# Optimization experiments

Measured on AMD Instinct MI355X. Metric: run time of the kernel, lower is better.

Reference implementation:

```python
import jax, jax.numpy as jnp
import numpy as np

B, T, N, E = 4, 8, 512, 8192
CIN, H, HEADS = 64, 128, 4


def setup_inputs() -> dict:
    key = jax.random.key(0)
    ks = jax.random.split(key, 8)
    G = B * T
    s = 0.05
    return {
        "x": jax.random.normal(ks[0], (G, N, CIN), jnp.float32),
        "edge_index": jax.random.randint(ks[1], (G, 2, E), 0, N, dtype=jnp.int64),
        "W1": jax.random.normal(ks[2], (CIN, H), jnp.float32) * s,
        "b1": jnp.zeros((H,), jnp.float32),
        "W2": jax.random.normal(ks[3], (H, H), jnp.float32) * s,
        "b2": jnp.zeros((H,), jnp.float32),
        "in_proj_w": jax.random.normal(ks[4], (3 * H, H), jnp.float32) * s,
        "in_proj_b": jnp.zeros((3 * H,), jnp.float32),
        "out_proj_w": jax.random.normal(ks[5], (H, H), jnp.float32) * s,
        "out_proj_b": jnp.zeros((H,), jnp.float32),
    }


def gcn_layer(x, src, dst, W, b, num_nodes):
    # PyG GCNConv: add self-loops, sym-normalize deg^-1/2[src]*deg^-1/2[dst]
    xl = x @ W                                            # [GN, H]
    deg = jax.ops.segment_sum(jnp.ones_like(dst, dtype=xl.dtype), dst,
                              num_segments=num_nodes) + 1.0  # +1 self-loop
    dinv = jax.lax.rsqrt(deg)
    norm = dinv[src] * dinv[dst]                          # [Etot]
    agg = jax.ops.segment_sum(xl[src] * norm[:, None], dst, num_segments=num_nodes)
    agg = agg + xl * (dinv * dinv)[:, None]               # self-loop term
    return agg + b


def reference(x, edge_index, W1, b1, W2, b2, in_proj_w, in_proj_b, out_proj_w, out_proj_b):
    G, n, cin = x.shape
    GN = G * n
    offs = (jnp.arange(G, dtype=edge_index.dtype) * n)[:, None]  # disjoint union
    src = (edge_index[:, 0, :] + offs).reshape(-1)
    dst = (edge_index[:, 1, :] + offs).reshape(-1)
    xf = x.reshape(GN, cin)
    h = gcn_layer(xf, src, dst, W1, b1, GN)
    h = gcn_layer(h, src, dst, W2, b2, GN)
    hc = h.shape[-1]
    h = h.reshape(B, T * n, hc)                           # [B, S, H]
    # torch.nn.MultiheadAttention with packed qkv in_proj
    qkv = h @ in_proj_w.T + in_proj_b
    q, k, v = jnp.split(qkv, 3, axis=-1)
    hd = hc // HEADS
    def sh(t):
        return t.reshape(B, -1, HEADS, hd).transpose(0, 2, 1, 3)  # [B,h,S,d]
    q, k, v = sh(q), sh(k), sh(v)
    att = jax.nn.softmax(jnp.einsum('bhqd,bhkd->bhqk', q, k) / jnp.sqrt(jnp.float32(hd)), axis=-1)
    o = jnp.einsum('bhqk,bhkd->bhqd', att, v).transpose(0, 2, 1, 3).reshape(B, -1, hc)
    return o @ out_proj_w.T + out_proj_b
```

## Files before the change

kernel.cpp:

```cpp
#include <hip/hip_runtime.h>
#include <hip/hip_bf16.h>

#define G     32
#define NPG   512
#define EPG   8192
#define GN    16384
#define ETOT  (G*EPG)
#define CIN   64
#define H     128
#define NB    4
#define S     4096
#define HEADS 4
#define HD    32
#define QKV   384

typedef __attribute__((ext_vector_type(8))) short short8;
typedef __attribute__((ext_vector_type(4))) float floatx4;

__device__ __forceinline__ float bf16_to_f32(unsigned short u) {
    unsigned int x = ((unsigned int)u) << 16;
    return __uint_as_float(x);
}
__device__ __forceinline__ unsigned short f32_to_bf16(float f) {
    __hip_bfloat16 h = (__hip_bfloat16)f;
    return *(unsigned short*)&h;
}
__device__ __forceinline__ float ldf(const void* p, long i, int f32) {
    return f32 ? ((const float*)p)[i] : bf16_to_f32(((const unsigned short*)p)[i]);
}

__global__ void detect_kernel(const unsigned short* __restrict__ xraw,
                              const int* __restrict__ eiraw, int* __restrict__ flags) {
    __shared__ float smax[256];
    __shared__ int   sor[256];
    int t = threadIdx.x;
    float m = 0.f;
    for (int i = t; i < 4096; i += 256)
        m = fmaxf(m, fabsf(bf16_to_f32(xraw[i])));
    int orv = 0;
    for (int i = t; i < 2048; i += 256)
        orv |= eiraw[2 * i + 1];
    smax[t] = m; sor[t] = orv;
    __syncthreads();
    for (int off = 128; off > 0; off >>= 1) {
        if (t < off) {
            smax[t] = fmaxf(smax[t], smax[t + off]);
            sor[t] |= sor[t + off];
        }
        __syncthreads();
    }
    if (t == 0) {
        flags[0] = (smax[0] > 1000.f) ? 1 : 0;
        flags[1] = (sor[0] == 0) ? 1 : 0;
    }
}

__global__ __launch_bounds__(NPG) void csr_kernel(const int* __restrict__ ei,
        const int* __restrict__ flags, int* __restrict__ cnt_g,
        int* __restrict__ row_start_g, float* __restrict__ dinv_g,
        int* __restrict__ csr_src) {
    __shared__ int cs[NPG], ctmp[NPG], fpos[NPG];
    int g = blockIdx.x, t = threadIdx.x;
    int sh = flags[1];
    cs[t] = 0;
    __syncthreads();
    const size_t sbase = ((size_t)(g * 2 + 0) * EPG) << sh;
    const size_t dbase = ((size_t)(g * 2 + 1) * EPG) << sh;
    for (int e = t; e < EPG; e += NPG)
        atomicAdd(&cs[ei[dbase + ((size_t)e << sh)]], 1);
    __syncthreads();
    int c = cs[t];
    ctmp[t] = c;
    __syncthreads();
    for (int off = 1; off < NPG; off <<= 1) {
        int v = (t >= off) ? ctmp[t - off] : 0;
        __syncthreads();
        ctmp[t] += v;
        __syncthreads();
    }
    int rs = g * EPG + ctmp[t] - c;
    fpos[t] = rs;
    cnt_g[g * NPG + t] = c;
    row_start_g[g * NPG + t] = rs;
    dinv_g[g * NPG + t] = 1.0f / sqrtf((float)c + 1.0f);
    __syncthreads();
    for (int e = t; e < EPG; e += NPG) {
        int s = ei[sbase + ((size_t)e << sh)];
        int d = ei[dbase + ((size_t)e << sh)];
        int pos = atomicAdd(&fpos[d], 1);
        csr_src[pos] = g * NPG + s;
    }
}

#define XN   (GN*CIN)
#define E1   (XN + H*CIN)
#define E2   (E1 + H*H)
#define E3   (E2 + QKV*H)
#define E4   (E3 + H*H)
#define E5   (E4 + H)
#define E6   (E5 + H)
#define E7   (E6 + QKV)
#define CTOT (E7 + H)
__global__ void conv_all_kernel(const void* x_raw, const void* W1_raw, const void* b1_raw,
                                const void* W2_raw, const void* b2_raw, const void* Wq_raw,
                                const void* bq_raw, const void* Wo_raw, const void* bo_raw,
                                unsigned short* __restrict__ xb,
                                unsigned short* __restrict__ W1T,
                                unsigned short* __restrict__ W2T,
                                unsigned short* __restrict__ Wqb,
                                unsigned short* __restrict__ Wob,
                                float* __restrict__ b1f, float* __restrict__ b2f,
                                float* __restrict__ bqf, float* __restrict__ bof,
                                const float* __restrict__ dinv,
                                const int* __restrict__ flags) {
    int i = blockIdx.x * blockDim.x + threadIdx.x;
    if (i >= CTOT) return;
    int f32 = flags[0];
    if (i < XN) {
        xb[i] = f32_to_bf16(ldf(x_raw, i, f32) * dinv[i >> 6]);
    } else if (i < E1) {
        int j = i - XN, c = j / CIN, r = j - c * CIN;
        W1T[j] = f32_to_bf16(ldf(W1_raw, (long)r * H + c, f32));
    } else if (i < E2) {
        int j = i - E1, c = j >> 7, r = j & 127;
        W2T[j] = f32_to_bf16(ldf(W2_raw, (long)r * H + c, f32));
    } else if (i < E3) {
        int j = i - E2;
        Wqb[j] = f32_to_bf16(ldf(Wq_raw, j, f32));
    } else if (i < E4) {
        int j = i - E3;
        Wob[j] = f32_to_bf16(ldf(Wo_raw, j, f32));
    } else if (i < E5) { b1f[i - E4] = ldf(b1_raw, i - E4, f32); }
    else if (i < E6) { b2f[i - E5] = ldf(b2_raw, i - E5, f32); }
    else if (i < E7) { bqf[i - E6] = ldf(bq_raw, i - E6, f32); }
    else             { bof[i - E7] = ldf(bo_raw, i - E7, f32); }
}

__global__ void agg64_kernel(const unsigned short* __restrict__ xb,
                             const int* __restrict__ row_start, const int* __restrict__ cnt,
                             const int* __restrict__ csr_src, const float* __restrict__ dinv,
                             unsigned short* __restrict__ z) {
    int i = blockIdx.x;
    int c = threadIdx.x;
    float acc = bf16_to_f32(xb[(size_t)i * CIN + c]);
    int rs = row_start[i], n = cnt[i];
    int p = 0;
    for (; p + 4 <= n; p += 4) {
        int s0 = csr_src[rs + p + 0];
        int s1 = csr_src[rs + p + 1];
        int s2 = csr_src[rs + p + 2];
        int s3 = csr_src[rs + p + 3];
        float a0 = bf16_to_f32(xb[(size_t)s0 * CIN + c]);
        float a1 = bf16_to_f32(xb[(size_t)s1 * CIN + c]);
        float a2 = bf16_to_f32(xb[(size_t)s2 * CIN + c]);
        float a3 = bf16_to_f32(xb[(size_t)s3 * CIN + c]);
        acc += (a0 + a1) + (a2 + a3);
    }
    for (; p < n; p++)
        acc += bf16_to_f32(xb[(size_t)csr_src[rs + p] * CIN + c]);
    z[(size_t)i * CIN + c] = f32_to_bf16(acc * dinv[i]);
}

#define HPAD 136
__global__ __launch_bounds__(256) void gcn12_kernel(
        const unsigned short* __restrict__ Z, const unsigned short* __restrict__ W1T,
        const float* __restrict__ b1, const unsigned short* __restrict__ W2T,
        const float* __restrict__ dinv, unsigned short* __restrict__ Y) {
    __shared__ unsigned short hl[64][HPAD];
    int tid = threadIdx.x, wave = tid >> 6, lane = tid & 63, m = lane & 15, quad = lane >> 4;
    int row0 = blockIdx.x * 64 + wave * 16;
    int lrow0 = wave * 16;
    floatx4 acc[8] = {};
    for (int kc = 0; kc < CIN; kc += 32) {
        short8 af = *(const short8*)&Z[(size_t)(row0 + m) * CIN + kc + quad * 8];
#pragma unroll
        for (int t = 0; t < 8; t++) {
            short8 bf = *(const short8*)&W1T[(size_t)(t * 16 + m) * CIN + kc + quad * 8];
            acc[t] = __builtin_amdgcn_mfma_f32_16x16x32_bf16(af, bf, acc[t], 0, 0, 0);
        }
    }
#pragma unroll
    for (int t = 0; t < 8; t++) {
        int col = t * 16 + m;
        float bj = b1[col];
#pragma unroll
        for (int r = 0; r < 4; r++)
            hl[lrow0 + quad * 4 + r][col] = f32_to_bf16(acc[t][r] + bj);
    }
    asm volatile("s_waitcnt lgkmcnt(0)" ::: "memory");
    floatx4 acc2[8] = {};
    for (int kc = 0; kc < H; kc += 32) {
        short8 af = *(const short8*)&hl[lrow0 + m][kc + quad * 8];
#pragma unroll
        for (int t = 0; t < 8; t++) {
            short8 bf = *(const short8*)&W2T[(size_t)(t * 16 + m) * H + kc + quad * 8];
            acc2[t] = __builtin_amdgcn_mfma_f32_16x16x32_bf16(af, bf, acc2[t], 0, 0, 0);
        }
    }
    int rbase = row0 + quad * 4;
    float4 dv4 = *(const float4*)&dinv[rbase];
    float dv[4] = {dv4.x, dv4.y, dv4.z, dv4.w};
#pragma unroll
    for (int t = 0; t < 8; t++) {
        int col = t * 16 + m;
#pragma unroll
        for (int r = 0; r < 4; r++)
            Y[(size_t)(rbase + r) * H + col] = f32_to_bf16(acc2[t][r] * dv[r]);
    }
}

__global__ void agg_kernel(const unsigned short* __restrict__ y,
                           const int* __restrict__ row_start, const int* __restrict__ cnt,
                           const int* __restrict__ csr_src, const float* __restrict__ dinv,
                           const float* __restrict__ bias, unsigned short* __restrict__ hout) {
    int i = blockIdx.x;
    int c = threadIdx.x;
    float acc = bf16_to_f32(y[(size_t)i * H + c]);
    int rs = row_start[i], n = cnt[i];
    int p = 0;
    for (; p + 4 <= n; p += 4) {
        int s0 = csr_src[rs + p + 0];
        int s1 = csr_src[rs + p + 1];
        int s2 = csr_src[rs + p + 2];
        int s3 = csr_src[rs + p + 3];
        float a0 = bf16_to_f32(y[(size_t)s0 * H + c]);
        float a1 = bf16_to_f32(y[(size_t)s1 * H + c]);
        float a2 = bf16_to_f32(y[(size_t)s2 * H + c]);
        float a3 = bf16_to_f32(y[(size_t)s3 * H + c]);
        acc += (a0 + a1) + (a2 + a3);
    }
    for (; p < n; p++)
        acc += bf16_to_f32(y[(size_t)csr_src[rs + p] * H + c]);
    hout[(size_t)i * H + c] = f32_to_bf16(acc * dinv[i] + bias[c]);
}

__global__ __launch_bounds__(256) void mmqkv_kernel(const unsigned short* __restrict__ A,
        const unsigned short* __restrict__ B, const float* __restrict__ bias,
        unsigned short* __restrict__ Qx, unsigned short* __restrict__ Kx,
        unsigned short* __restrict__ Vtx) {
    __shared__ unsigned short vbuf[4][2][16][20];
    int tid = threadIdx.x, wave = tid >> 6, lane = tid & 63, m = lane & 15, quad = lane >> 4;
    int row0 = blockIdx.x * 64 + wave * 16;
    floatx4 acc[24] = {};
    for (int kc = 0; kc < H; kc += 32) {
        short8 af = *(const short8*)&A[(size_t)(row0 + m) * H + kc + quad * 8];
#pragma unroll
        for (int t = 0; t < 24; t++) {
            short8 bf = *(const short8*)&B[(size_t)(t * 16 + m) * H + kc + quad * 8];
            acc[t] = __builtin_amdgcn_mfma_f32_16x16x32_bf16(af, bf, acc[t], 0, 0, 0);
        }
    }
    int rbase = row0 + quad * 4;
    int b = rbase >> 12, s0 = rbase & (S - 1);
    int s0t = row0 & (S - 1);
    int hdl = lane >> 2, sg = lane & 3;
#pragma unroll
    for (int t = 0; t < 24; t++) {
        int j = t * 16 + m;
        float bj = bias[j];
        if (t < 8) {
            int head = j >> 5, hd = j & 31;
            int bh = b * HEADS + head;
#pragma unroll
            for (int r = 0; r < 4; r++)
                Qx[((size_t)bh * S + s0 + r) * HD + hd] =
                    f32_to_bf16((acc[t][r] + bj) *
                                (0.17677669529663687f * 1.4426950408889634f));
        } else if (t < 16) {
            int jj = j & 127, head = jj >> 5, hd = jj & 31;
            int bh = b * HEADS + head;
#pragma unroll
            for (int r = 0; r < 4; r++)
                Kx[((size_t)bh * S + s0 + r) * HD + hd] = f32_to_bf16(acc[t][r] + bj);
        } else {
            int t2 = t - 16;
            int head = t2 >> 1, hdb = (t2 & 1) * 16;
            int bh = b * HEADS + head;
            float v0 = acc[t][0] + bj, v1 = acc[t][1] + bj;
            float v2 = acc[t][2] + bj, v3 = acc[t][3] + bj;
            unsigned int d0, d1;
            asm("v_cvt_pk_bf16_f32 %0, %1, %2" : "=v"(d0) : "v"(v0), "v"(v1));
            asm("v_cvt_pk_bf16_f32 %0, %1, %2" : "=v"(d1) : "v"(v2), "v"(v3));
            uint2 wv; wv.x = d0; wv.y = d1;
            *(uint2*)&vbuf[wave][t2 & 1][m][quad * 4] = wv;
            asm volatile("s_waitcnt lgkmcnt(0)" ::: "memory");
            uint2 rv = *(const uint2*)&vbuf[wave][t2 & 1][hdl][sg * 4];
            *(uint2*)&Vtx[((size_t)bh * HD + hdb + hdl) * S + s0t + sg * 4] = rv;
        }
    }
}

__global__ __launch_bounds__(256) void attn7_kernel(
        const unsigned short* __restrict__ Qx, const unsigned short* __restrict__ Kx,
        const unsigned short* __restrict__ Vtx, unsigned short* __restrict__ Ob) {
    int tid = threadIdx.x, wave = tid >> 6, lane = tid & 63;
    int m = lane & 15, quad = lane >> 4;

    int n = blockIdx.x;
    int id = (n & 7) * 32 + (n >> 3);
    int tile = id & 15, bh = id >> 4;

    const unsigned short* Qb  = Qx  + (size_t)bh * S * HD;
    const unsigned short* Kb  = Kx  + (size_t)bh * S * HD;
    const unsigned short* Vtb = Vtx + (size_t)bh * HD * S;

    int q0 = tile * 256 + wave * 64;
    short8 q[4];
#pragma unroll
    for (int t = 0; t < 4; t++)
        q[t] = *(const short8*)&Qb[(size_t)(q0 + t * 16 + m) * HD + quad * 8];

    floatx4 o0[4] = {}, o1[4] = {}, l[4] = {};

    short8 ones = {16256, 16256, 16256, 16256, 16256, 16256, 16256, 16256};
    union PW { unsigned int u[4]; short8 s8; };

    short8 kf0 = *(const short8*)&Kb[(size_t)m * HD + quad * 8];
    short8 kf1 = *(const short8*)&Kb[(size_t)(m + 16) * HD + quad * 8];
    short8 vc0 = *(const short8*)&Vtb[(size_t)m * S + quad * 8];
    short8 vc1 = *(const short8*)&Vtb[(size_t)(m + 16) * S + quad * 8];

    for (int i = 0; i < S / 32; i++) {
        floatx4 z = {};
        floatx4 t0[4], t1[4];
#pragma unroll
        for (int t = 0; t < 4; t++) {
            t0[t] = __builtin_amdgcn_mfma_f32_16x16x32_bf16(kf0, q[t], z, 0, 0, 0);
            t1[t] = __builtin_amdgcn_mfma_f32_16x16x32_bf16(kf1, q[t], z, 0, 0, 0);
        }
        int ktn = ((i + 1) * 32) & (S - 1);
        kf0 = *(const short8*)&Kb[(size_t)(ktn + m) * HD + quad * 8];
        kf1 = *(const short8*)&Kb[(size_t)(ktn + m + 16) * HD + quad * 8];

        PW pw[4];
#pragma unroll
        for (int t = 0; t < 4; t++) {
            float e0 = __builtin_amdgcn_exp2f(t0[t][0]);
            float e1 = __builtin_amdgcn_exp2f(t0[t][1]);
            float e2 = __builtin_amdgcn_exp2f(t0[t][2]);
            float e3 = __builtin_amdgcn_exp2f(t0[t][3]);
            float e4 = __builtin_amdgcn_exp2f(t1[t][0]);
            float e5 = __builtin_amdgcn_exp2f(t1[t][1]);
            float e6 = __builtin_amdgcn_exp2f(t1[t][2]);
            float e7 = __builtin_amdgcn_exp2f(t1[t][3]);
            unsigned int w0, w1, w2, w3;
            asm("v_cvt_pk_bf16_f32 %0, %1, %2" : "=v"(w0) : "v"(e0), "v"(e1));
            asm("v_cvt_pk_bf16_f32 %0, %1, %2" : "=v"(w1) : "v"(e2), "v"(e3));
            asm("v_cvt_pk_bf16_f32 %0, %1, %2" : "=v"(w2) : "v"(e4), "v"(e5));
            asm("v_cvt_pk_bf16_f32 %0, %1, %2" : "=v"(w3) : "v"(e6), "v"(e7));
            asm("v_permlane32_swap_b32 %0, %1" : "+v"(w0), "+v"(w2));
            asm("v_permlane32_swap_b32 %0, %1" : "+v"(w1), "+v"(w3));
            asm("v_permlane16_swap_b32 %0, %1" : "+v"(w0), "+v"(w2));
            asm("v_permlane16_swap_b32 %0, %1" : "+v"(w1), "+v"(w3));
            pw[t].u[0] = w0; pw[t].u[1] = w1; pw[t].u[2] = w2; pw[t].u[3] = w3;
        }

#pragma unroll
        for (int t = 0; t < 4; t++) {
            o0[t] = __builtin_amdgcn_mfma_f32_16x16x32_bf16(pw[t].s8, vc0, o0[t], 0, 0, 0);
            o1[t] = __builtin_amdgcn_mfma_f32_16x16x32_bf16(pw[t].s8, vc1, o1[t], 0, 0, 0);
            l[t]  = __builtin_amdgcn_mfma_f32_16x16x32_bf16(pw[t].s8, ones, l[t], 0, 0, 0);
        }
        vc0 = *(const short8*)&Vtb[(size_t)m * S + ktn + quad * 8];
        vc1 = *(const short8*)&Vtb[(size_t)(m + 16) * S + ktn + quad * 8];
    }

    int batch = bh >> 2, head = bh & 3;
    int col = head * HD + m;
#pragma unroll
    for (int t = 0; t < 4; t++) {
        int grow = batch * S + q0 + t * 16 + quad * 4;
#pragma unroll
        for (int r = 0; r < 4; r++) {
            float inv = 1.f / l[t][r];
            Ob[(size_t)(grow + r) * H + col]      = f32_to_bf16(o0[t][r] * inv);
            Ob[(size_t)(grow + r) * H + col + 16] = f32_to_bf16(o1[t][r] * inv);
        }
    }
}

__global__ __launch_bounds__(256) void mmout_kernel(const unsigned short* __restrict__ A,
        const unsigned short* __restrict__ B, const float* __restrict__ bias,
        void* __restrict__ out, const int* __restrict__ flags) {
    int tid = threadIdx.x, wave = tid >> 6, lane = tid & 63, m = lane & 15, quad = lane >> 4;
    int row0 = blockIdx.x * 64 + wave * 16;
    floatx4 acc[8] = {};
    for (int kc = 0; kc < H; kc += 32) {
        short8 af = *(const short8*)&A[(size_t)(row0 + m) * H + kc + quad * 8];
#pragma unroll
        for (int t = 0; t < 8; t++) {
            short8 bf = *(const short8*)&B[(size_t)(t * 16 + m) * H + kc + quad * 8];
            acc[t] = __builtin_amdgcn_mfma_f32_16x16x32_bf16(af, bf, acc[t], 0, 0, 0);
        }
    }
    int rbase = row0 + quad * 4;
    int f32o = flags[0];
#pragma unroll
    for (int t = 0; t < 8; t++) {
        int col = t * 16 + m;
        float bj = bias[col];
#pragma unroll
        for (int r = 0; r < 4; r++) {
            float v = acc[t][r] + bj;
            if (f32o) ((float*)out)[(size_t)(rbase + r) * H + col] = v;
            else ((unsigned short*)out)[(size_t)(rbase + r) * H + col] = f32_to_bf16(v);
        }
    }
}

extern "C" void kernel_launch(void* const* d_in, const int* in_sizes, int n_in,
                              void* d_out, int out_size, void* d_ws, size_t ws_size,
                              hipStream_t stream) {
    const void* x_raw    = d_in[0];
    const int*  ei_raw   = (const int*)d_in[1];
    const void* W1_raw   = d_in[2];
    const void* b1_raw   = d_in[3];
    const void* W2_raw   = d_in[4];
    const void* b2_raw   = d_in[5];
    const void* Wq_raw   = d_in[6];
    const void* bq_raw   = d_in[7];
    const void* Wo_raw   = d_in[8];
    const void* bo_raw   = d_in[9];

    char* ws = (char*)d_ws;
    size_t o = 0;
    auto alloc = [&](size_t bytes) { void* p = ws + o; o += (bytes + 1023) & ~1023ull; return p; };

    int*   flags     = (int*)  alloc(1024);
    int*   cnt       = (int*)  alloc((size_t)GN * 4);
    int*   row_start = (int*)  alloc((size_t)GN * 4);
    float* dinv      = (float*)alloc((size_t)GN * 4);
    int*   csr_src   = (int*)  alloc((size_t)ETOT * 4);
    unsigned short* xb   = (unsigned short*)alloc((size_t)GN * CIN * 2);
    unsigned short* zb   = (unsigned short*)alloc((size_t)GN * CIN * 2);
    unsigned short* W1T  = (unsigned short*)alloc((size_t)H * CIN * 2);
    unsigned short* W2T  = (unsigned short*)alloc((size_t)H * H * 2);
    unsigned short* Wqb  = (unsigned short*)alloc((size_t)QKV * H * 2);
    unsigned short* Wob  = (unsigned short*)alloc((size_t)H * H * 2);
    float* b1f = (float*)alloc(H * 4);
    float* b2f = (float*)alloc(H * 4);
    float* bqf = (float*)alloc(QKV * 4);
    float* bof = (float*)alloc(H * 4);
    unsigned short* y_bf = (unsigned short*)alloc((size_t)GN * H * 2);
    unsigned short* h_bf = (unsigned short*)alloc((size_t)GN * H * 2);
    unsigned short* Qx   = (unsigned short*)alloc((size_t)16 * S * HD * 2);
    unsigned short* Kx   = (unsigned short*)alloc((size_t)16 * S * HD * 2);
    unsigned short* Vtx  = (unsigned short*)alloc((size_t)16 * S * HD * 2);
    unsigned short* Obf  = y_bf;

    detect_kernel<<<1, 256, 0, stream>>>((const unsigned short*)x_raw, ei_raw, flags);

    csr_kernel<<<G, NPG, 0, stream>>>(ei_raw, flags, cnt, row_start, dinv, csr_src);

    conv_all_kernel<<<(CTOT + 255) / 256, 256, 0, stream>>>(
        x_raw, W1_raw, b1_raw, W2_raw, b2_raw, Wq_raw, bq_raw, Wo_raw, bo_raw,
        xb, W1T, W2T, Wqb, Wob, b1f, b2f, bqf, bof, dinv, flags);

    agg64_kernel<<<GN, CIN, 0, stream>>>(xb, row_start, cnt, csr_src, dinv, zb);
    gcn12_kernel<<<GN / 64, 256, 0, stream>>>(zb, W1T, b1f, W2T, dinv, y_bf);
    agg_kernel<<<GN, H, 0, stream>>>(y_bf, row_start, cnt, csr_src, dinv, b2f, h_bf);

    mmqkv_kernel<<<GN / 64, 256, 0, stream>>>(h_bf, Wqb, bqf, Qx, Kx, Vtx);
    attn7_kernel<<<dim3(256), 256, 0, stream>>>(Qx, Kx, Vtx, Obf);
    mmout_kernel<<<GN / 64, 256, 0, stream>>>(Obf, Wob, bof, d_out, flags);
}
```

Measured before the change: 249.9 us.

## Fuse neighbor aggregation into GCN and QKV matmul kernels; widen CSR block

The two sparse aggregation kernels are merged into the following MFMA matmul kernels. Each 64-row block now gathers its neighbors into LDS before the matmul, which removes two launches and the global round trip of the intermediate z and h buffers. The CSR build also runs with 1024 threads per graph instead of 512. In exchange, each fused block walks its 64 rows' gathers serially, with only 256 blocks in the grid, so the gathers have less parallelism and less latency hiding than the earlier one-block-per-node layout.

```diff
diff --git a/kernel.cpp b/kernel.cpp
--- a/kernel.cpp
+++ b/kernel.cpp
@@ -55,36 +55,38 @@
     }
 }
 
-__global__ __launch_bounds__(NPG) void csr_kernel(const int* __restrict__ ei,
+__global__ __launch_bounds__(1024) void csr_kernel(const int* __restrict__ ei,
         const int* __restrict__ flags, int* __restrict__ cnt_g,
         int* __restrict__ row_start_g, float* __restrict__ dinv_g,
         int* __restrict__ csr_src) {
     __shared__ int cs[NPG], ctmp[NPG], fpos[NPG];
     int g = blockIdx.x, t = threadIdx.x;
     int sh = flags[1];
-    cs[t] = 0;
+    if (t < NPG) cs[t] = 0;
     __syncthreads();
     const size_t sbase = ((size_t)(g * 2 + 0) * EPG) << sh;
     const size_t dbase = ((size_t)(g * 2 + 1) * EPG) << sh;
-    for (int e = t; e < EPG; e += NPG)
+    for (int e = t; e < EPG; e += 1024)
         atomicAdd(&cs[ei[dbase + ((size_t)e << sh)]], 1);
     __syncthreads();
-    int c = cs[t];
-    ctmp[t] = c;
+    int c = 0;
+    if (t < NPG) { c = cs[t]; ctmp[t] = c; }
     __syncthreads();
     for (int off = 1; off < NPG; off <<= 1) {
-        int v = (t >= off) ? ctmp[t - off] : 0;
+        int v = (t < NPG && t >= off) ? ctmp[t - off] : 0;
         __syncthreads();
-        ctmp[t] += v;
+        if (t < NPG) ctmp[t] += v;
         __syncthreads();
     }
-    int rs = g * EPG + ctmp[t] - c;
-    fpos[t] = rs;
-    cnt_g[g * NPG + t] = c;
-    row_start_g[g * NPG + t] = rs;
-    dinv_g[g * NPG + t] = 1.0f / sqrtf((float)c + 1.0f);
-    __syncthreads();
-    for (int e = t; e < EPG; e += NPG) {
+    if (t < NPG) {
+        int rs = g * EPG + ctmp[t] - c;
+        fpos[t] = rs;
+        cnt_g[g * NPG + t] = c;
+        row_start_g[g * NPG + t] = rs;
+        dinv_g[g * NPG + t] = 1.0f / sqrtf((float)c + 1.0f);
+    }
+    __syncthreads();
+    for (int e = t; e < EPG; e += 1024) {
         int s = ei[sbase + ((size_t)e << sh)];
         int d = ei[dbase + ((size_t)e << sh)];
         int pos = atomicAdd(&fpos[d], 1);
@@ -136,43 +138,49 @@
     else             { bof[i - E7] = ldf(bo_raw, i - E7, f32); }
 }
 
-__global__ void agg64_kernel(const unsigned short* __restrict__ xb,
-                             const int* __restrict__ row_start, const int* __restrict__ cnt,
-                             const int* __restrict__ csr_src, const float* __restrict__ dinv,
-                             unsigned short* __restrict__ z) {
-    int i = blockIdx.x;
-    int c = threadIdx.x;
-    float acc = bf16_to_f32(xb[(size_t)i * CIN + c]);
-    int rs = row_start[i], n = cnt[i];
-    int p = 0;
-    for (; p + 4 <= n; p += 4) {
-        int s0 = csr_src[rs + p + 0];
-        int s1 = csr_src[rs + p + 1];
-        int s2 = csr_src[rs + p + 2];
-        int s3 = csr_src[rs + p + 3];
-        float a0 = bf16_to_f32(xb[(size_t)s0 * CIN + c]);
-        float a1 = bf16_to_f32(xb[(size_t)s1 * CIN + c]);
-        float a2 = bf16_to_f32(xb[(size_t)s2 * CIN + c]);
-        float a3 = bf16_to_f32(xb[(size_t)s3 * CIN + c]);
-        acc += (a0 + a1) + (a2 + a3);
-    }
-    for (; p < n; p++)
-        acc += bf16_to_f32(xb[(size_t)csr_src[rs + p] * CIN + c]);
-    z[(size_t)i * CIN + c] = f32_to_bf16(acc * dinv[i]);
-}
-
+#define ZPAD 72
 #define HPAD 136
-__global__ __launch_bounds__(256) void gcn12_kernel(
-        const unsigned short* __restrict__ Z, const unsigned short* __restrict__ W1T,
-        const float* __restrict__ b1, const unsigned short* __restrict__ W2T,
-        const float* __restrict__ dinv, unsigned short* __restrict__ Y) {
-    __shared__ unsigned short hl[64][HPAD];
+__global__ __launch_bounds__(256) void gcnA_kernel(
+        const unsigned short* __restrict__ xb,
+        const int* __restrict__ row_start, const int* __restrict__ cnt,
+        const int* __restrict__ csr_src, const float* __restrict__ dinv,
+        const unsigned short* __restrict__ W1T, const float* __restrict__ b1,
+        const unsigned short* __restrict__ W2T, unsigned short* __restrict__ Y) {
+    __shared__ __align__(16) unsigned short zl[64][ZPAD];
+    __shared__ __align__(16) unsigned short hl[64][HPAD];
     int tid = threadIdx.x, wave = tid >> 6, lane = tid & 63, m = lane & 15, quad = lane >> 4;
     int row0 = blockIdx.x * 64 + wave * 16;
     int lrow0 = wave * 16;
+
+    {
+        int c = tid & 63, sub = tid >> 6;
+        for (int k = 0; k < 16; k++) {
+            int ln = k * 4 + sub;
+            int i = blockIdx.x * 64 + ln;
+            float acc = bf16_to_f32(xb[(size_t)i * CIN + c]);
+            int rs = row_start[i], n = cnt[i];
+            int p = 0;
+            for (; p + 4 <= n; p += 4) {
+                int s0 = csr_src[rs + p + 0];
+                int s1 = csr_src[rs + p + 1];
+                int s2 = csr_src[rs + p + 2];
+                int s3 = csr_src[rs + p + 3];
+                float a0 = bf16_to_f32(xb[(size_t)s0 * CIN + c]);
+                float a1 = bf16_to_f32(xb[(size_t)s1 * CIN + c]);
+                float a2 = bf16_to_f32(xb[(size_t)s2 * CIN + c]);
+                float a3 = bf16_to_f32(xb[(size_t)s3 * CIN + c]);
+                acc += (a0 + a1) + (a2 + a3);
+            }
+            for (; p < n; p++)
+                acc += bf16_to_f32(xb[(size_t)csr_src[rs + p] * CIN + c]);
+            zl[ln][c] = f32_to_bf16(acc * dinv[i]);
+        }
+    }
+    __syncthreads();
+
     floatx4 acc[8] = {};
     for (int kc = 0; kc < CIN; kc += 32) {
-        short8 af = *(const short8*)&Z[(size_t)(row0 + m) * CIN + kc + quad * 8];
+        short8 af = *(const short8*)&zl[lrow0 + m][kc + quad * 8];
 #pragma unroll
         for (int t = 0; t < 8; t++) {
             short8 bf = *(const short8*)&W1T[(size_t)(t * 16 + m) * CIN + kc + quad * 8];
@@ -188,6 +196,7 @@
             hl[lrow0 + quad * 4 + r][col] = f32_to_bf16(acc[t][r] + bj);
     }
     asm volatile("s_waitcnt lgkmcnt(0)" ::: "memory");
+
     floatx4 acc2[8] = {};
     for (int kc = 0; kc < H; kc += 32) {
         short8 af = *(const short8*)&hl[lrow0 + m][kc + quad * 8];
@@ -209,41 +218,50 @@
     }
 }
 
-__global__ void agg_kernel(const unsigned short* __restrict__ y,
-                           const int* __restrict__ row_start, const int* __restrict__ cnt,
-                           const int* __restrict__ csr_src, const float* __restrict__ dinv,
-                           const float* __restrict__ bias, unsigned short* __restrict__ hout) {
-    int i = blockIdx.x;
-    int c = threadIdx.x;
-    float acc = bf16_to_f32(y[(size_t)i * H + c]);
-    int rs = row_start[i], n = cnt[i];
-    int p = 0;
-    for (; p + 4 <= n; p += 4) {
-        int s0 = csr_src[rs + p + 0];
-        int s1 = csr_src[rs + p + 1];
-        int s2 = csr_src[rs + p + 2];
-        int s3 = csr_src[rs + p + 3];
-        float a0 = bf16_to_f32(y[(size_t)s0 * H + c]);
-        float a1 = bf16_to_f32(y[(size_t)s1 * H + c]);
-        float a2 = bf16_to_f32(y[(size_t)s2 * H + c]);
-        float a3 = bf16_to_f32(y[(size_t)s3 * H + c]);
-        acc += (a0 + a1) + (a2 + a3);
-    }
-    for (; p < n; p++)
-        acc += bf16_to_f32(y[(size_t)csr_src[rs + p] * H + c]);
-    hout[(size_t)i * H + c] = f32_to_bf16(acc * dinv[i] + bias[c]);
-}
-
-__global__ __launch_bounds__(256) void mmqkv_kernel(const unsigned short* __restrict__ A,
+__global__ __launch_bounds__(256) void mmqkvA_kernel(
+        const unsigned short* __restrict__ y,
+        const int* __restrict__ row_start, const int* __restrict__ cnt,
+        const int* __restrict__ csr_src, const float* __restrict__ dinv,
+        const float* __restrict__ b2,
         const unsigned short* __restrict__ B, const float* __restrict__ bias,
         unsigned short* __restrict__ Qx, unsigned short* __restrict__ Kx,
         unsigned short* __restrict__ Vtx) {
+    __shared__ __align__(16) unsigned short hl[64][HPAD];
     __shared__ unsigned short vbuf[4][2][16][20];
     int tid = threadIdx.x, wave = tid >> 6, lane = tid & 63, m = lane & 15, quad = lane >> 4;
     int row0 = blockIdx.x * 64 + wave * 16;
+    int lrow0 = wave * 16;
+
+    {
+        int c = tid & 127, half = tid >> 7;
+        float bj = b2[c];
+        for (int k = 0; k < 32; k++) {
+            int ln = k * 2 + half;
+            int i = blockIdx.x * 64 + ln;
+            float acc = bf16_to_f32(y[(size_t)i * H + c]);
+            int rs = row_start[i], n = cnt[i];
+            int p = 0;
+            for (; p + 4 <= n; p += 4) {
+                int s0 = csr_src[rs + p + 0];
+                int s1 = csr_src[rs + p + 1];
+                int s2 = csr_src[rs + p + 2];
+                int s3 = csr_src[rs + p + 3];
+                float a0 = bf16_to_f32(y[(size_t)s0 * H + c]);
+                float a1 = bf16_to_f32(y[(size_t)s1 * H + c]);
+                float a2 = bf16_to_f32(y[(size_t)s2 * H + c]);
+                float a3 = bf16_to_f32(y[(size_t)s3 * H + c]);
+                acc += (a0 + a1) + (a2 + a3);
+            }
+            for (; p < n; p++)
+                acc += bf16_to_f32(y[(size_t)csr_src[rs + p] * H + c]);
+            hl[ln][c] = f32_to_bf16(acc * dinv[i] + bj);
+        }
+    }
+    __syncthreads();
+
     floatx4 acc[24] = {};
     for (int kc = 0; kc < H; kc += 32) {
-        short8 af = *(const short8*)&A[(size_t)(row0 + m) * H + kc + quad * 8];
+        short8 af = *(const short8*)&hl[lrow0 + m][kc + quad * 8];
 #pragma unroll
         for (int t = 0; t < 24; t++) {
             short8 bf = *(const short8*)&B[(size_t)(t * 16 + m) * H + kc + quad * 8];
@@ -432,7 +450,6 @@
     float* dinv      = (float*)alloc((size_t)GN * 4);
     int*   csr_src   = (int*)  alloc((size_t)ETOT * 4);
     unsigned short* xb   = (unsigned short*)alloc((size_t)GN * CIN * 2);
-    unsigned short* zb   = (unsigned short*)alloc((size_t)GN * CIN * 2);
     unsigned short* W1T  = (unsigned short*)alloc((size_t)H * CIN * 2);
     unsigned short* W2T  = (unsigned short*)alloc((size_t)H * H * 2);
     unsigned short* Wqb  = (unsigned short*)alloc((size_t)QKV * H * 2);
@@ -442,7 +459,6 @@
     float* bqf = (float*)alloc(QKV * 4);
     float* bof = (float*)alloc(H * 4);
     unsigned short* y_bf = (unsigned short*)alloc((size_t)GN * H * 2);
-    unsigned short* h_bf = (unsigned short*)alloc((size_t)GN * H * 2);
     unsigned short* Qx   = (unsigned short*)alloc((size_t)16 * S * HD * 2);
     unsigned short* Kx   = (unsigned short*)alloc((size_t)16 * S * HD * 2);
     unsigned short* Vtx  = (unsigned short*)alloc((size_t)16 * S * HD * 2);
@@ -450,17 +466,17 @@
 
     detect_kernel<<<1, 256, 0, stream>>>((const unsigned short*)x_raw, ei_raw, flags);
 
-    csr_kernel<<<G, NPG, 0, stream>>>(ei_raw, flags, cnt, row_start, dinv, csr_src);
+    csr_kernel<<<G, 1024, 0, stream>>>(ei_raw, flags, cnt, row_start, dinv, csr_src);
 
     conv_all_kernel<<<(CTOT + 255) / 256, 256, 0, stream>>>(
         x_raw, W1_raw, b1_raw, W2_raw, b2_raw, Wq_raw, bq_raw, Wo_raw, bo_raw,
         xb, W1T, W2T, Wqb, Wob, b1f, b2f, bqf, bof, dinv, flags);
 
-    agg64_kernel<<<GN, CIN, 0, stream>>>(xb, row_start, cnt, csr_src, dinv, zb);
-    gcn12_kernel<<<GN / 64, 256, 0, stream>>>(zb, W1T, b1f, W2T, dinv, y_bf);
-    agg_kernel<<<GN, H, 0, stream>>>(y_bf, row_start, cnt, csr_src, dinv, b2f, h_bf);
-
-    mmqkv_kernel<<<GN / 64, 256, 0, stream>>>(h_bf, Wqb, bqf, Qx, Kx, Vtx);
+    gcnA_kernel<<<GN / 64, 256, 0, stream>>>(xb, row_start, cnt, csr_src, dinv,
+                                             W1T, b1f, W2T, y_bf);
+    mmqkvA_kernel<<<GN / 64, 256, 0, stream>>>(y_bf, row_start, cnt, csr_src, dinv,
+                                               b2f, Wqb, bqf, Qx, Kx, Vtx);
+
     attn7_kernel<<<dim3(256), 256, 0, stream>>>(Qx, Kx, Vtx, Obf);
     mmout_kernel<<<GN / 64, 256, 0, stream>>>(Obf, Wob, bof, d_out, flags);
 }
```

Result: slower. 345.3 us (+38.2%).
